# Performance work log

Measured on AMD Instinct MI355X. Metric: run time of the kernel, lower is better.

Reference implementation:

```python
import jax, jax.numpy as jnp
import numpy as np

N_NODES = 500000
N_GRAPHS = 4096
D_LOCAL = 64
D_GLOBAL = 64
D_HIDDEN = 128
D_PRE = 64
LN_EPS = 1e-5


def _layer_norm(x, g, b):
    mu = jnp.mean(x, axis=-1, keepdims=True)
    var = jnp.var(x, axis=-1, keepdims=True)
    return (x - mu) * jax.lax.rsqrt(var + LN_EPS) * g + b


def setup_inputs() -> dict:
    key = jax.random.key(0)
    ks = jax.random.split(key, 16)
    s = 0.02
    d_concat = D_LOCAL + D_GLOBAL  # 128
    d_post_in = D_PRE + D_GLOBAL   # 128
    return {
        "x": jax.random.normal(ks[0], (N_NODES, D_LOCAL), jnp.float32),
        "u": jax.random.normal(ks[1], (N_GRAPHS, D_GLOBAL), jnp.float32),
        "batch": jax.random.randint(ks[2], (N_NODES,), 0, N_GRAPHS, jnp.int64),
        # mlp_pre_aggr params
        "w1": jax.random.normal(ks[3], (d_concat, D_HIDDEN), jnp.float32) * s,
        "b1": jnp.zeros((D_HIDDEN,), jnp.float32),
        "w2": jax.random.normal(ks[4], (D_HIDDEN, D_HIDDEN), jnp.float32) * s,
        "b2": jnp.zeros((D_HIDDEN,), jnp.float32),
        "w3": jax.random.normal(ks[5], (D_HIDDEN, D_PRE), jnp.float32) * s,
        "b3": jnp.zeros((D_PRE,), jnp.float32),
        "ln1_g": jnp.ones((D_PRE,), jnp.float32),
        "ln1_b": jnp.zeros((D_PRE,), jnp.float32),
        # mlp_post_aggr params
        "w4": jax.random.normal(ks[6], (d_post_in, D_HIDDEN), jnp.float32) * s,
        "b4": jnp.zeros((D_HIDDEN,), jnp.float32),
        "w5": jax.random.normal(ks[7], (D_HIDDEN, D_HIDDEN), jnp.float32) * s,
        "b5": jnp.zeros((D_HIDDEN,), jnp.float32),
        "w6": jax.random.normal(ks[8], (D_HIDDEN, D_GLOBAL), jnp.float32) * s,
        "b6": jnp.zeros((D_GLOBAL,), jnp.float32),
        "ln2_g": jnp.ones((D_GLOBAL,), jnp.float32),
        "ln2_b": jnp.zeros((D_GLOBAL,), jnp.float32),
    }


def reference(x, u, batch, w1, b1, w2, b2, w3, b3, ln1_g, ln1_b,
              w4, b4, w5, b5, w6, b6, ln2_g, ln2_b):
    # gather global state to nodes and concat: [N, dim_local + dim_global]
    h = jnp.concatenate([x, u[batch]], axis=-1)
    # mlp_pre_aggr (dropout p=0 -> identity)
    h = jax.nn.relu(h @ w1 + b1)
    h = jax.nn.relu(h @ w2 + b2)
    h = _layer_norm(h @ w3 + b3, ln1_g, ln1_b)  # [N, dim_pre_aggr]
    # scatter_add per graph
    agg = jax.ops.segment_sum(h, batch, num_segments=u.shape[0])  # [B, dim_pre_aggr]
    # concat with u, mlp_post_aggr
    g = jnp.concatenate([agg, u], axis=-1)
    g = jax.nn.relu(g @ w4 + b4)
    g = jax.nn.relu(g @ w5 + b5)
    g = _layer_norm(g @ w6 + b6, ln2_g, ln2_b)
    return g + u
```

## Files before the change

kernel.cpp:

```cpp
#include <hip/hip_runtime.h>
#include <hip/hip_bf16.h>
#include <stdint.h>


#define NNODES 500000
#define NGRAPHS 4096
#define ROWS 128
#define LDH 136

typedef __attribute__((ext_vector_type(8))) _Float16 half8;
typedef __attribute__((ext_vector_type(4))) float floatx4;

__global__ void prep_kernel(const float* __restrict__ w1, const float* __restrict__ w2,
                            const float* __restrict__ w3,
                            _Float16* __restrict__ w1T, _Float16* __restrict__ w2T,
                            _Float16* __restrict__ w3T) {
    int i = blockIdx.x * 256 + threadIdx.x;
    if (i < 128 * 128) {
        int n = i >> 7, k = i & 127;
        w1T[i] = (_Float16)w1[k * 128 + n];
        w2T[i] = (_Float16)w2[k * 128 + n];
    }
    if (i < 64 * 128) {
        int n = i >> 7, k = i & 127;
        w3T[i] = (_Float16)w3[k * 64 + n];
    }
}

__global__ __launch_bounds__(256, 2) void node_kernel(
    const float* __restrict__ x, const float* __restrict__ u, const int* __restrict__ batch,
    const _Float16* __restrict__ w1T, const _Float16* __restrict__ w2T,
    const _Float16* __restrict__ w3T,
    const float* __restrict__ b1, const float* __restrict__ b2, const float* __restrict__ b3,
    const float* __restrict__ lng, const float* __restrict__ lnb,
    float* __restrict__ agg)
{
    __shared__ __align__(16) _Float16 hA[ROWS * LDH];
    __shared__ int sBatch[ROWS];

    const int tid = threadIdx.x;
    const int rowbase = blockIdx.x * ROWS;
    const int wave = tid >> 6;
    const int lane = tid & 63;
    const int q = lane >> 4;
    const int l16 = lane & 15;

    for (int r = tid; r < ROWS; r += 256) {
        int gr = rowbase + r;
        sBatch[r] = (gr < NNODES) ? batch[gr] : 0;
    }
    __syncthreads();

    for (int i = tid; i < ROWS * 16; i += 256) {
        int r = i >> 4, c4 = (i & 15) << 2;
        int gr = rowbase + r;
        float4 vx = make_float4(0.f, 0.f, 0.f, 0.f);
        if (gr < NNODES) vx = *(const float4*)(x + (size_t)gr * 64 + c4);
        _Float16* p = &hA[r * LDH + c4];
        p[0] = (_Float16)vx.x; p[1] = (_Float16)vx.y;
        p[2] = (_Float16)vx.z; p[3] = (_Float16)vx.w;
        int g = sBatch[r];
        float4 vu = *(const float4*)(u + (size_t)g * 64 + c4);
        _Float16* p2 = &hA[r * LDH + 64 + c4];
        p2[0] = (_Float16)vu.x; p2[1] = (_Float16)vu.y;
        p2[2] = (_Float16)vu.z; p2[3] = (_Float16)vu.w;
    }
    __syncthreads();

    const int rowg = (wave >> 1) * 64;
    const int colg = (wave & 1) * 64;
    for (int layer = 0; layer < 2; ++layer) {
        const _Float16* wT = layer ? w2T : w1T;
        const float* bias = layer ? b2 : b1;
        floatx4 acc[4][4];
        #pragma unroll
        for (int ct = 0; ct < 4; ++ct) {
            float bv = bias[colg + ct * 16 + l16];
            #pragma unroll
            for (int rt = 0; rt < 4; ++rt) acc[rt][ct] = (floatx4){bv, bv, bv, bv};
        }
        half8 bfr[4][4];
        #pragma unroll
        for (int ks = 0; ks < 4; ++ks)
            #pragma unroll
            for (int ct = 0; ct < 4; ++ct)
                bfr[ks][ct] = *(const half8*)(wT + (colg + ct * 16 + l16) * 128 + ks * 32 + q * 8);
        #pragma unroll
        for (int ks = 0; ks < 4; ++ks) {
            half8 af[4];
            #pragma unroll
            for (int rt = 0; rt < 4; ++rt)
                af[rt] = *(const half8*)(&hA[(rowg + rt * 16 + l16) * LDH + ks * 32 + q * 8]);
            #pragma unroll
            for (int rt = 0; rt < 4; ++rt)
                #pragma unroll
                for (int ct = 0; ct < 4; ++ct)
                    acc[rt][ct] = __builtin_amdgcn_mfma_f32_16x16x32_f16(
                        af[rt], bfr[ks][ct], acc[rt][ct], 0, 0, 0);
        }
        __syncthreads();
        #pragma unroll
        for (int rt = 0; rt < 4; ++rt)
            #pragma unroll
            for (int ct = 0; ct < 4; ++ct)
                #pragma unroll
                for (int j = 0; j < 4; ++j) {
                    float v = acc[rt][ct][j];
                    v = v > 0.f ? v : 0.f;
                    hA[(rowg + rt * 16 + q * 4 + j) * LDH + colg + ct * 16 + l16] = (_Float16)v;
                }
        __syncthreads();
    }

    {
        const int rowg3 = wave * 32;
        floatx4 acc[2][4];
        #pragma unroll
        for (int ct = 0; ct < 4; ++ct) {
            float bv = b3[ct * 16 + l16];
            acc[0][ct] = (floatx4){bv, bv, bv, bv};
            acc[1][ct] = (floatx4){bv, bv, bv, bv};
        }
        half8 bfr[4][4];
        #pragma unroll
        for (int ks = 0; ks < 4; ++ks)
            #pragma unroll
            for (int ct = 0; ct < 4; ++ct)
                bfr[ks][ct] = *(const half8*)(w3T + (ct * 16 + l16) * 128 + ks * 32 + q * 8);
        #pragma unroll
        for (int ks = 0; ks < 4; ++ks) {
            half8 af[2];
            #pragma unroll
            for (int rt = 0; rt < 2; ++rt)
                af[rt] = *(const half8*)(&hA[(rowg3 + rt * 16 + l16) * LDH + ks * 32 + q * 8]);
            #pragma unroll
            for (int rt = 0; rt < 2; ++rt)
                #pragma unroll
                for (int ct = 0; ct < 4; ++ct)
                    acc[rt][ct] = __builtin_amdgcn_mfma_f32_16x16x32_f16(
                        af[rt], bfr[ks][ct], acc[rt][ct], 0, 0, 0);
        }
        float gct[4], bct[4];
        #pragma unroll
        for (int ct = 0; ct < 4; ++ct) {
            gct[ct] = lng[ct * 16 + l16];
            bct[ct] = lnb[ct * 16 + l16];
        }
        #pragma unroll
        for (int rt = 0; rt < 2; ++rt)
            #pragma unroll
            for (int j = 0; j < 4; ++j) {
                int rloc = rowg3 + rt * 16 + q * 4 + j;
                float v0 = acc[rt][0][j], v1 = acc[rt][1][j];
                float v2 = acc[rt][2][j], v3 = acc[rt][3][j];
                float s = v0 + v1 + v2 + v3;
                float ss = v0 * v0 + v1 * v1 + v2 * v2 + v3 * v3;
                #pragma unroll
                for (int m = 1; m < 16; m <<= 1) {
                    s += __shfl_xor(s, m, 16);
                    ss += __shfl_xor(ss, m, 16);
                }
                float mean = s * (1.f / 64.f);
                float var = ss * (1.f / 64.f) - mean * mean;
                float rstd = rsqrtf(var + 1e-5f);
                if (rowbase + rloc < NNODES) {
                    float* dst = agg + (size_t)sBatch[rloc] * 64;
                    unsafeAtomicAdd(dst + 0 + l16,  (v0 - mean) * rstd * gct[0] + bct[0]);
                    unsafeAtomicAdd(dst + 16 + l16, (v1 - mean) * rstd * gct[1] + bct[1]);
                    unsafeAtomicAdd(dst + 32 + l16, (v2 - mean) * rstd * gct[2] + bct[2]);
                    unsafeAtomicAdd(dst + 48 + l16, (v3 - mean) * rstd * gct[3] + bct[3]);
                }
            }
    }
}

__global__ __launch_bounds__(256, 4) void graph_kernel(
    const float* __restrict__ u,
    const float* __restrict__ w4, const float* __restrict__ b4,
    const float* __restrict__ w5, const float* __restrict__ b5,
    const float* __restrict__ w6, const float* __restrict__ b6,
    const float* __restrict__ g2, const float* __restrict__ bb2,
    float* __restrict__ out)
{
    __shared__ float z[4][2][128];
    const int wave = threadIdx.x >> 6, lane = threadIdx.x & 63;
    const int g = blockIdx.x * 4 + wave;
    float* za = z[wave][0];
    float* zb = z[wave][1];
    za[lane] = out[(size_t)g * 64 + lane];
    za[64 + lane] = u[(size_t)g * 64 + lane];
    float s0 = b4[lane], s1 = b4[64 + lane];
    for (int k = 0; k < 128; ++k) {
        float zk = za[k];
        s0 = fmaf(zk, w4[k * 128 + lane], s0);
        s1 = fmaf(zk, w4[k * 128 + 64 + lane], s1);
    }
    zb[lane] = fmaxf(s0, 0.f); zb[64 + lane] = fmaxf(s1, 0.f);
    s0 = b5[lane]; s1 = b5[64 + lane];
    for (int k = 0; k < 128; ++k) {
        float zk = zb[k];
        s0 = fmaf(zk, w5[k * 128 + lane], s0);
        s1 = fmaf(zk, w5[k * 128 + 64 + lane], s1);
    }
    za[lane] = fmaxf(s0, 0.f); za[64 + lane] = fmaxf(s1, 0.f);
    float s = b6[lane];
    for (int k = 0; k < 128; ++k) s = fmaf(za[k], w6[k * 64 + lane], s);
    float sum = s, ssq = s * s;
    #pragma unroll
    for (int m = 1; m < 64; m <<= 1) {
        sum += __shfl_xor(sum, m, 64);
        ssq += __shfl_xor(ssq, m, 64);
    }
    float mean = sum * (1.f / 64.f);
    float var = ssq * (1.f / 64.f) - mean * mean;
    float rstd = rsqrtf(var + 1e-5f);
    out[(size_t)g * 64 + lane] =
        (s - mean) * rstd * g2[lane] + bb2[lane] + u[(size_t)g * 64 + lane];
}

extern "C" void kernel_launch(void* const* d_in, const int* in_sizes, int n_in,
                              void* d_out, int out_size, void* d_ws, size_t ws_size,
                              hipStream_t stream) {
    const float* x   = (const float*)d_in[0];
    const float* u   = (const float*)d_in[1];
    const int*   bt  = (const int*)d_in[2];
    const float* w1  = (const float*)d_in[3];
    const float* b1  = (const float*)d_in[4];
    const float* w2  = (const float*)d_in[5];
    const float* b2  = (const float*)d_in[6];
    const float* w3  = (const float*)d_in[7];
    const float* b3  = (const float*)d_in[8];
    const float* lng = (const float*)d_in[9];
    const float* lnb = (const float*)d_in[10];
    const float* w4  = (const float*)d_in[11];
    const float* b4  = (const float*)d_in[12];
    const float* w5  = (const float*)d_in[13];
    const float* b5  = (const float*)d_in[14];
    const float* w6  = (const float*)d_in[15];
    const float* b6  = (const float*)d_in[16];
    const float* g2  = (const float*)d_in[17];
    const float* bb2 = (const float*)d_in[18];
    float* out = (float*)d_out;

    _Float16* w1T = (_Float16*)d_ws;
    _Float16* w2T = w1T + 128 * 128;
    _Float16* w3T = w2T + 128 * 128;

    hipMemsetAsync(d_out, 0, (size_t)NGRAPHS * 64 * sizeof(float), stream);
    prep_kernel<<<64, 256, 0, stream>>>(w1, w2, w3, w1T, w2T, w3T);
    node_kernel<<<(NNODES + ROWS - 1) / ROWS, 256, 0, stream>>>(
        x, u, bt, w1T, w2T, w3T, b1, b2, b3, lng, lnb, out);
    graph_kernel<<<NGRAPHS / 4, 256, 0, stream>>>(
        u, w4, b4, w5, b5, w6, b6, g2, bb2, out);
}
```

Before: 408.0 us.

## Sort nodes by graph for LDS-local segment sums and MFMA the graph MLP

Adds a histogram, scan and scatter pass that builds a permutation grouping nodes by graph id. The node kernel then gathers x through that permutation, so each 128-row block spans only a few graphs and can accumulate its segment sums in shared-memory slots before one global atomic flush per slot. This is meant to cut the heavy contention of per-row global float atomics. The per-graph post-aggregation MLP is also rewritten to use fp16 MFMA tiles with transposed half-precision weights, replacing the scalar FMA loops. The cost is three extra kernel launches, a scattered gather of x rows, and lower precision in the graph MLP.

```diff
diff --git a/kernel.cpp b/kernel.cpp
--- a/kernel.cpp
+++ b/kernel.cpp
@@ -7,28 +7,79 @@
 #define NGRAPHS 4096
 #define ROWS 128
 #define LDH 136
+#define SLOTS 16
 
 typedef __attribute__((ext_vector_type(8))) _Float16 half8;
 typedef __attribute__((ext_vector_type(4))) float floatx4;
 
 __global__ void prep_kernel(const float* __restrict__ w1, const float* __restrict__ w2,
-                            const float* __restrict__ w3,
+                            const float* __restrict__ w3, const float* __restrict__ w4,
+                            const float* __restrict__ w5, const float* __restrict__ w6,
                             _Float16* __restrict__ w1T, _Float16* __restrict__ w2T,
-                            _Float16* __restrict__ w3T) {
+                            _Float16* __restrict__ w3T, _Float16* __restrict__ w4T,
+                            _Float16* __restrict__ w5T, _Float16* __restrict__ w6T) {
     int i = blockIdx.x * 256 + threadIdx.x;
     if (i < 128 * 128) {
         int n = i >> 7, k = i & 127;
         w1T[i] = (_Float16)w1[k * 128 + n];
         w2T[i] = (_Float16)w2[k * 128 + n];
+        w4T[i] = (_Float16)w4[k * 128 + n];
+        w5T[i] = (_Float16)w5[k * 128 + n];
     }
     if (i < 64 * 128) {
         int n = i >> 7, k = i & 127;
         w3T[i] = (_Float16)w3[k * 64 + n];
+        w6T[i] = (_Float16)w6[k * 64 + n];
+    }
+}
+
+__global__ void hist_kernel(const int* __restrict__ batch, int* __restrict__ cnt) {
+    __shared__ int h[NGRAPHS];
+    for (int i = threadIdx.x; i < NGRAPHS; i += 256) h[i] = 0;
+    __syncthreads();
+    for (int i = blockIdx.x * 256 + threadIdx.x; i < NNODES; i += 64 * 256)
+        atomicAdd(&h[batch[i]], 1);
+    __syncthreads();
+    for (int i = threadIdx.x; i < NGRAPHS; i += 256) {
+        int v = h[i];
+        if (v) atomicAdd(&cnt[i], v);
+    }
+}
+
+__global__ void scan_kernel(const int* __restrict__ cnt, int* __restrict__ runoff) {
+    __shared__ int partial[256];
+    int tid = threadIdx.x;
+    int local[16];
+    int s = 0;
+    #pragma unroll
+    for (int j = 0; j < 16; ++j) { local[j] = cnt[tid * 16 + j]; s += local[j]; }
+    partial[tid] = s;
+    __syncthreads();
+    for (int off = 1; off < 256; off <<= 1) {
+        int v = (tid >= off) ? partial[tid - off] : 0;
+        __syncthreads();
+        partial[tid] += v;
+        __syncthreads();
+    }
+    int run = partial[tid] - s;
+    #pragma unroll
+    for (int j = 0; j < 16; ++j) { runoff[tid * 16 + j] = run; run += local[j]; }
+}
+
+__global__ void scatter_kernel(const int* __restrict__ batch, int* __restrict__ runoff,
+                               int* __restrict__ perm, int* __restrict__ sbat) {
+    int i = blockIdx.x * 256 + threadIdx.x;
+    if (i < NNODES) {
+        int g = batch[i];
+        int p = atomicAdd(&runoff[g], 1);
+        perm[p] = i;
+        sbat[p] = g;
     }
 }
 
 __global__ __launch_bounds__(256, 2) void node_kernel(
-    const float* __restrict__ x, const float* __restrict__ u, const int* __restrict__ batch,
+    const float* __restrict__ x, const float* __restrict__ u,
+    const int* __restrict__ perm, const int* __restrict__ sbat,
     const _Float16* __restrict__ w1T, const _Float16* __restrict__ w2T,
     const _Float16* __restrict__ w3T,
     const float* __restrict__ b1, const float* __restrict__ b2, const float* __restrict__ b3,
@@ -37,6 +88,8 @@
 {
     __shared__ __align__(16) _Float16 hA[ROWS * LDH];
     __shared__ int sBatch[ROWS];
+    __shared__ int sPerm[ROWS];
+    __shared__ float aggS[SLOTS * 64];
 
     const int tid = threadIdx.x;
     const int rowbase = blockIdx.x * ROWS;
@@ -47,15 +100,22 @@
 
     for (int r = tid; r < ROWS; r += 256) {
         int gr = rowbase + r;
-        sBatch[r] = (gr < NNODES) ? batch[gr] : 0;
-    }
-    __syncthreads();
+        sPerm[r] = (gr < NNODES) ? perm[gr] : -1;
+        sBatch[r] = (gr < NNODES) ? sbat[gr] : 0;
+    }
+    for (int i = tid; i < SLOTS * 64; i += 256) aggS[i] = 0.f;
+    __syncthreads();
+
+    const int nValid = (rowbase + ROWS <= NNODES) ? ROWS : (NNODES - rowbase);
+    const int gFirst = sBatch[0];
+    const int nSlots = sBatch[nValid - 1] - gFirst + 1;
+    const bool useLds = (nSlots <= SLOTS);
 
     for (int i = tid; i < ROWS * 16; i += 256) {
         int r = i >> 4, c4 = (i & 15) << 2;
-        int gr = rowbase + r;
+        int nid = sPerm[r];
         float4 vx = make_float4(0.f, 0.f, 0.f, 0.f);
-        if (gr < NNODES) vx = *(const float4*)(x + (size_t)gr * 64 + c4);
+        if (nid >= 0) vx = *(const float4*)(x + (size_t)nid * 64 + c4);
         _Float16* p = &hA[r * LDH + c4];
         p[0] = (_Float16)vx.x; p[1] = (_Float16)vx.y;
         p[2] = (_Float16)vx.z; p[3] = (_Float16)vx.w;
@@ -164,58 +224,167 @@
                 float var = ss * (1.f / 64.f) - mean * mean;
                 float rstd = rsqrtf(var + 1e-5f);
                 if (rowbase + rloc < NNODES) {
-                    float* dst = agg + (size_t)sBatch[rloc] * 64;
-                    unsafeAtomicAdd(dst + 0 + l16,  (v0 - mean) * rstd * gct[0] + bct[0]);
-                    unsafeAtomicAdd(dst + 16 + l16, (v1 - mean) * rstd * gct[1] + bct[1]);
-                    unsafeAtomicAdd(dst + 32 + l16, (v2 - mean) * rstd * gct[2] + bct[2]);
-                    unsafeAtomicAdd(dst + 48 + l16, (v3 - mean) * rstd * gct[3] + bct[3]);
+                    float o0 = (v0 - mean) * rstd * gct[0] + bct[0];
+                    float o1 = (v1 - mean) * rstd * gct[1] + bct[1];
+                    float o2 = (v2 - mean) * rstd * gct[2] + bct[2];
+                    float o3 = (v3 - mean) * rstd * gct[3] + bct[3];
+                    if (useLds) {
+                        float* dst = aggS + (sBatch[rloc] - gFirst) * 64;
+                        atomicAdd(dst + 0 + l16,  o0);
+                        atomicAdd(dst + 16 + l16, o1);
+                        atomicAdd(dst + 32 + l16, o2);
+                        atomicAdd(dst + 48 + l16, o3);
+                    } else {
+                        float* dst = agg + (size_t)sBatch[rloc] * 64;
+                        unsafeAtomicAdd(dst + 0 + l16,  o0);
+                        unsafeAtomicAdd(dst + 16 + l16, o1);
+                        unsafeAtomicAdd(dst + 32 + l16, o2);
+                        unsafeAtomicAdd(dst + 48 + l16, o3);
+                    }
                 }
             }
     }
-}
-
-__global__ __launch_bounds__(256, 4) void graph_kernel(
+    __syncthreads();
+    if (useLds) {
+        for (int i = tid; i < nSlots * 64; i += 256)
+            unsafeAtomicAdd(agg + (size_t)(gFirst + (i >> 6)) * 64 + (i & 63), aggS[i]);
+    }
+}
+
+__global__ __launch_bounds__(256, 2) void graph2_kernel(
     const float* __restrict__ u,
-    const float* __restrict__ w4, const float* __restrict__ b4,
-    const float* __restrict__ w5, const float* __restrict__ b5,
-    const float* __restrict__ w6, const float* __restrict__ b6,
-    const float* __restrict__ g2, const float* __restrict__ bb2,
+    const _Float16* __restrict__ w4T, const _Float16* __restrict__ w5T,
+    const _Float16* __restrict__ w6T,
+    const float* __restrict__ b4, const float* __restrict__ b5, const float* __restrict__ b6,
+    const float* __restrict__ lng, const float* __restrict__ lnb,
     float* __restrict__ out)
 {
-    __shared__ float z[4][2][128];
-    const int wave = threadIdx.x >> 6, lane = threadIdx.x & 63;
-    const int g = blockIdx.x * 4 + wave;
-    float* za = z[wave][0];
-    float* zb = z[wave][1];
-    za[lane] = out[(size_t)g * 64 + lane];
-    za[64 + lane] = u[(size_t)g * 64 + lane];
-    float s0 = b4[lane], s1 = b4[64 + lane];
-    for (int k = 0; k < 128; ++k) {
-        float zk = za[k];
-        s0 = fmaf(zk, w4[k * 128 + lane], s0);
-        s1 = fmaf(zk, w4[k * 128 + 64 + lane], s1);
-    }
-    zb[lane] = fmaxf(s0, 0.f); zb[64 + lane] = fmaxf(s1, 0.f);
-    s0 = b5[lane]; s1 = b5[64 + lane];
-    for (int k = 0; k < 128; ++k) {
-        float zk = zb[k];
-        s0 = fmaf(zk, w5[k * 128 + lane], s0);
-        s1 = fmaf(zk, w5[k * 128 + 64 + lane], s1);
-    }
-    za[lane] = fmaxf(s0, 0.f); za[64 + lane] = fmaxf(s1, 0.f);
-    float s = b6[lane];
-    for (int k = 0; k < 128; ++k) s = fmaf(za[k], w6[k * 64 + lane], s);
-    float sum = s, ssq = s * s;
-    #pragma unroll
-    for (int m = 1; m < 64; m <<= 1) {
-        sum += __shfl_xor(sum, m, 64);
-        ssq += __shfl_xor(ssq, m, 64);
-    }
-    float mean = sum * (1.f / 64.f);
-    float var = ssq * (1.f / 64.f) - mean * mean;
-    float rstd = rsqrtf(var + 1e-5f);
-    out[(size_t)g * 64 + lane] =
-        (s - mean) * rstd * g2[lane] + bb2[lane] + u[(size_t)g * 64 + lane];
+    __shared__ __align__(16) _Float16 hA[128 * LDH];
+
+    const int tid = threadIdx.x;
+    const int rowbase = blockIdx.x * 128;
+    const int wave = tid >> 6;
+    const int lane = tid & 63;
+    const int q = lane >> 4;
+    const int l16 = lane & 15;
+
+    for (int i = tid; i < 128 * 16; i += 256) {
+        int r = i >> 4, c4 = (i & 15) << 2;
+        int g = rowbase + r;
+        float4 va = *(const float4*)(out + (size_t)g * 64 + c4);
+        _Float16* p = &hA[r * LDH + c4];
+        p[0] = (_Float16)va.x; p[1] = (_Float16)va.y;
+        p[2] = (_Float16)va.z; p[3] = (_Float16)va.w;
+        float4 vu = *(const float4*)(u + (size_t)g * 64 + c4);
+        _Float16* p2 = &hA[r * LDH + 64 + c4];
+        p2[0] = (_Float16)vu.x; p2[1] = (_Float16)vu.y;
+        p2[2] = (_Float16)vu.z; p2[3] = (_Float16)vu.w;
+    }
+    __syncthreads();
+
+    const int rowg = (wave >> 1) * 64;
+    const int colg = (wave & 1) * 64;
+    for (int layer = 0; layer < 2; ++layer) {
+        const _Float16* wT = layer ? w5T : w4T;
+        const float* bias = layer ? b5 : b4;
+        floatx4 acc[4][4];
+        #pragma unroll
+        for (int ct = 0; ct < 4; ++ct) {
+            float bv = bias[colg + ct * 16 + l16];
+            #pragma unroll
+            for (int rt = 0; rt < 4; ++rt) acc[rt][ct] = (floatx4){bv, bv, bv, bv};
+        }
+        half8 bfr[4][4];
+        #pragma unroll
+        for (int ks = 0; ks < 4; ++ks)
+            #pragma unroll
+            for (int ct = 0; ct < 4; ++ct)
+                bfr[ks][ct] = *(const half8*)(wT + (colg + ct * 16 + l16) * 128 + ks * 32 + q * 8);
+        #pragma unroll
+        for (int ks = 0; ks < 4; ++ks) {
+            half8 af[4];
+            #pragma unroll
+            for (int rt = 0; rt < 4; ++rt)
+                af[rt] = *(const half8*)(&hA[(rowg + rt * 16 + l16) * LDH + ks * 32 + q * 8]);
+            #pragma unroll
+            for (int rt = 0; rt < 4; ++rt)
+                #pragma unroll
+                for (int ct = 0; ct < 4; ++ct)
+                    acc[rt][ct] = __builtin_amdgcn_mfma_f32_16x16x32_f16(
+                        af[rt], bfr[ks][ct], acc[rt][ct], 0, 0, 0);
+        }
+        __syncthreads();
+        #pragma unroll
+        for (int rt = 0; rt < 4; ++rt)
+            #pragma unroll
+            for (int ct = 0; ct < 4; ++ct)
+                #pragma unroll
+                for (int j = 0; j < 4; ++j) {
+                    float v = acc[rt][ct][j];
+                    v = v > 0.f ? v : 0.f;
+                    hA[(rowg + rt * 16 + q * 4 + j) * LDH + colg + ct * 16 + l16] = (_Float16)v;
+                }
+        __syncthreads();
+    }
+
+    {
+        const int rowg3 = wave * 32;
+        floatx4 acc[2][4];
+        #pragma unroll
+        for (int ct = 0; ct < 4; ++ct) {
+            float bv = b6[ct * 16 + l16];
+            acc[0][ct] = (floatx4){bv, bv, bv, bv};
+            acc[1][ct] = (floatx4){bv, bv, bv, bv};
+        }
+        half8 bfr[4][4];
+        #pragma unroll
+        for (int ks = 0; ks < 4; ++ks)
+            #pragma unroll
+            for (int ct = 0; ct < 4; ++ct)
+                bfr[ks][ct] = *(const half8*)(w6T + (ct * 16 + l16) * 128 + ks * 32 + q * 8);
+        #pragma unroll
+        for (int ks = 0; ks < 4; ++ks) {
+            half8 af[2];
+            #pragma unroll
+            for (int rt = 0; rt < 2; ++rt)
+                af[rt] = *(const half8*)(&hA[(rowg3 + rt * 16 + l16) * LDH + ks * 32 + q * 8]);
+            #pragma unroll
+            for (int rt = 0; rt < 2; ++rt)
+                #pragma unroll
+                for (int ct = 0; ct < 4; ++ct)
+                    acc[rt][ct] = __builtin_amdgcn_mfma_f32_16x16x32_f16(
+                        af[rt], bfr[ks][ct], acc[rt][ct], 0, 0, 0);
+        }
+        float gct[4], bct[4];
+        #pragma unroll
+        for (int ct = 0; ct < 4; ++ct) {
+            gct[ct] = lng[ct * 16 + l16];
+            bct[ct] = lnb[ct * 16 + l16];
+        }
+        #pragma unroll
+        for (int rt = 0; rt < 2; ++rt)
+            #pragma unroll
+            for (int j = 0; j < 4; ++j) {
+                int rloc = rowg3 + rt * 16 + q * 4 + j;
+                size_t g = (size_t)(rowbase + rloc);
+                float v0 = acc[rt][0][j], v1 = acc[rt][1][j];
+                float v2 = acc[rt][2][j], v3 = acc[rt][3][j];
+                float s = v0 + v1 + v2 + v3;
+                float ss = v0 * v0 + v1 * v1 + v2 * v2 + v3 * v3;
+                #pragma unroll
+                for (int m = 1; m < 16; m <<= 1) {
+                    s += __shfl_xor(s, m, 16);
+                    ss += __shfl_xor(ss, m, 16);
+                }
+                float mean = s * (1.f / 64.f);
+                float var = ss * (1.f / 64.f) - mean * mean;
+                float rstd = rsqrtf(var + 1e-5f);
+                out[g * 64 + 0 + l16]  = (v0 - mean) * rstd * gct[0] + bct[0] + u[g * 64 + 0 + l16];
+                out[g * 64 + 16 + l16] = (v1 - mean) * rstd * gct[1] + bct[1] + u[g * 64 + 16 + l16];
+                out[g * 64 + 32 + l16] = (v2 - mean) * rstd * gct[2] + bct[2] + u[g * 64 + 32 + l16];
+                out[g * 64 + 48 + l16] = (v3 - mean) * rstd * gct[3] + bct[3] + u[g * 64 + 48 + l16];
+            }
+    }
 }
 
 extern "C" void kernel_launch(void* const* d_in, const int* in_sizes, int n_in,
@@ -245,11 +414,23 @@
     _Float16* w1T = (_Float16*)d_ws;
     _Float16* w2T = w1T + 128 * 128;
     _Float16* w3T = w2T + 128 * 128;
+    _Float16* w4T = w3T + 64 * 128;
+    _Float16* w5T = w4T + 128 * 128;
+    _Float16* w6T = w5T + 128 * 128;
+    int* cnt    = (int*)(w6T + 64 * 128);
+    int* runoff = cnt + NGRAPHS;
+    int* perm   = runoff + NGRAPHS;
+    int* sbat   = perm + NNODES;
 
     hipMemsetAsync(d_out, 0, (size_t)NGRAPHS * 64 * sizeof(float), stream);
-    prep_kernel<<<64, 256, 0, stream>>>(w1, w2, w3, w1T, w2T, w3T);
+    hipMemsetAsync(cnt, 0, (size_t)NGRAPHS * sizeof(int), stream);
+    prep_kernel<<<64, 256, 0, stream>>>(w1, w2, w3, w4, w5, w6,
+                                        w1T, w2T, w3T, w4T, w5T, w6T);
+    hist_kernel<<<64, 256, 0, stream>>>(bt, cnt);
+    scan_kernel<<<1, 256, 0, stream>>>(cnt, runoff);
+    scatter_kernel<<<(NNODES + 255) / 256, 256, 0, stream>>>(bt, runoff, perm, sbat);
     node_kernel<<<(NNODES + ROWS - 1) / ROWS, 256, 0, stream>>>(
-        x, u, bt, w1T, w2T, w3T, b1, b2, b3, lng, lnb, out);
-    graph_kernel<<<NGRAPHS / 4, 256, 0, stream>>>(
-        u, w4, b4, w5, b5, w6, b6, g2, bb2, out);
-}
+        x, u, perm, sbat, w1T, w2T, w3T, b1, b2, b3, lng, lnb, out);
+    graph2_kernel<<<NGRAPHS / 128, 256, 0, stream>>>(
+        u, w4T, w5T, w6T, b4, b5, b6, g2, bb2, out);
+}
```

Result: slower. 532.4 us (+30.5%).

## Restructure node MLP to per-wave 32-row tiles and MFMA graph MLP

Applied to the files above, without the earlier changes.

The node kernel now gives each wave its own 32-row tile in shared memory and drops the block-wide __syncthreads. It reads weight fragments from global/L2 inside the loop instead of holding them in registers, which targets higher occupancy (4 blocks per CU). The graph-level MLP moves from a scalar FMA kernel to an fp16 MFMA kernel modelled on the node kernel, with w4-w6 transposed in prep. The risks are more repeated weight loads per wave and fp16 precision in the post-aggregation MLP. The graph kernel reads the aggregate from out and overwrites it in place per block.

```diff
diff --git a/kernel.cpp b/kernel.cpp
--- a/kernel.cpp
+++ b/kernel.cpp
@@ -5,61 +5,179 @@
 
 #define NNODES 500000
 #define NGRAPHS 4096
-#define ROWS 128
 #define LDH 136
 
 typedef __attribute__((ext_vector_type(8))) _Float16 half8;
 typedef __attribute__((ext_vector_type(4))) float floatx4;
 
 __global__ void prep_kernel(const float* __restrict__ w1, const float* __restrict__ w2,
-                            const float* __restrict__ w3,
+                            const float* __restrict__ w3, const float* __restrict__ w4,
+                            const float* __restrict__ w5, const float* __restrict__ w6,
                             _Float16* __restrict__ w1T, _Float16* __restrict__ w2T,
-                            _Float16* __restrict__ w3T) {
+                            _Float16* __restrict__ w3T, _Float16* __restrict__ w4T,
+                            _Float16* __restrict__ w5T, _Float16* __restrict__ w6T) {
     int i = blockIdx.x * 256 + threadIdx.x;
     if (i < 128 * 128) {
         int n = i >> 7, k = i & 127;
         w1T[i] = (_Float16)w1[k * 128 + n];
         w2T[i] = (_Float16)w2[k * 128 + n];
+        w4T[i] = (_Float16)w4[k * 128 + n];
+        w5T[i] = (_Float16)w5[k * 128 + n];
     }
     if (i < 64 * 128) {
         int n = i >> 7, k = i & 127;
         w3T[i] = (_Float16)w3[k * 64 + n];
+        w6T[i] = (_Float16)w6[k * 64 + n];
     }
 }
 
-__global__ __launch_bounds__(256, 2) void node_kernel(
-    const float* __restrict__ x, const float* __restrict__ u, const int* __restrict__ batch,
+__global__ __launch_bounds__(256, 4) void node_kernel(
+    const float* __restrict__ x, const float* __restrict__ u,
+    const int* __restrict__ batch,
     const _Float16* __restrict__ w1T, const _Float16* __restrict__ w2T,
     const _Float16* __restrict__ w3T,
     const float* __restrict__ b1, const float* __restrict__ b2, const float* __restrict__ b3,
     const float* __restrict__ lng, const float* __restrict__ lnb,
     float* __restrict__ agg)
 {
-    __shared__ __align__(16) _Float16 hA[ROWS * LDH];
-    __shared__ int sBatch[ROWS];
+    __shared__ __align__(16) _Float16 hA[4][32 * LDH];
 
     const int tid = threadIdx.x;
-    const int rowbase = blockIdx.x * ROWS;
     const int wave = tid >> 6;
     const int lane = tid & 63;
     const int q = lane >> 4;
     const int l16 = lane & 15;
-
-    for (int r = tid; r < ROWS; r += 256) {
+    const int wid = blockIdx.x * 4 + wave;
+    const int rowbase = wid * 32;
+    if (rowbase >= NNODES) return;
+    _Float16* hw = hA[wave];
+
+    float gct[4], bct[4];
+    #pragma unroll
+    for (int ct = 0; ct < 4; ++ct) {
+        gct[ct] = lng[ct * 16 + l16];
+        bct[ct] = lnb[ct * 16 + l16];
+    }
+
+    #pragma unroll
+    for (int k = 0; k < 16; ++k) {
+        int c = lane + k * 64;
+        int r = c >> 5;
+        int cc = c & 31;
         int gr = rowbase + r;
-        sBatch[r] = (gr < NNODES) ? batch[gr] : 0;
-    }
-    __syncthreads();
-
-    for (int i = tid; i < ROWS * 16; i += 256) {
+        float4 v;
+        if (cc < 16) {
+            v = *(const float4*)(x + (size_t)gr * 64 + cc * 4);
+        } else {
+            int g = batch[gr];
+            v = *(const float4*)(u + (size_t)g * 64 + (cc - 16) * 4);
+        }
+        _Float16* p = &hw[r * LDH + cc * 4];
+        p[0] = (_Float16)v.x; p[1] = (_Float16)v.y;
+        p[2] = (_Float16)v.z; p[3] = (_Float16)v.w;
+    }
+
+    for (int layer = 0; layer < 2; ++layer) {
+        const _Float16* wT = layer ? w2T : w1T;
+        const float* bias = layer ? b2 : b1;
+        #pragma unroll
+        for (int rt = 0; rt < 2; ++rt) {
+            half8 af[4];
+            #pragma unroll
+            for (int ks = 0; ks < 4; ++ks)
+                af[ks] = *(const half8*)(&hw[(rt * 16 + l16) * LDH + ks * 32 + q * 8]);
+            floatx4 acc[8];
+            #pragma unroll
+            for (int ct = 0; ct < 8; ++ct) {
+                float bv = bias[ct * 16 + l16];
+                acc[ct] = (floatx4){bv, bv, bv, bv};
+            }
+            #pragma unroll
+            for (int ct = 0; ct < 8; ++ct)
+                #pragma unroll
+                for (int ks = 0; ks < 4; ++ks) {
+                    half8 bf = *(const half8*)(wT + (ct * 16 + l16) * 128 + ks * 32 + q * 8);
+                    acc[ct] = __builtin_amdgcn_mfma_f32_16x16x32_f16(af[ks], bf, acc[ct], 0, 0, 0);
+                }
+            #pragma unroll
+            for (int ct = 0; ct < 8; ++ct)
+                #pragma unroll
+                for (int j = 0; j < 4; ++j) {
+                    float v = acc[ct][j];
+                    v = v > 0.f ? v : 0.f;
+                    hw[(rt * 16 + q * 4 + j) * LDH + ct * 16 + l16] = (_Float16)v;
+                }
+        }
+    }
+
+    #pragma unroll
+    for (int rt = 0; rt < 2; ++rt) {
+        half8 af[4];
+        #pragma unroll
+        for (int ks = 0; ks < 4; ++ks)
+            af[ks] = *(const half8*)(&hw[(rt * 16 + l16) * LDH + ks * 32 + q * 8]);
+        floatx4 acc[4];
+        #pragma unroll
+        for (int ct = 0; ct < 4; ++ct) {
+            float bv = b3[ct * 16 + l16];
+            acc[ct] = (floatx4){bv, bv, bv, bv};
+        }
+        #pragma unroll
+        for (int ct = 0; ct < 4; ++ct)
+            #pragma unroll
+            for (int ks = 0; ks < 4; ++ks) {
+                half8 bf = *(const half8*)(w3T + (ct * 16 + l16) * 128 + ks * 32 + q * 8);
+                acc[ct] = __builtin_amdgcn_mfma_f32_16x16x32_f16(af[ks], bf, acc[ct], 0, 0, 0);
+            }
+        #pragma unroll
+        for (int j = 0; j < 4; ++j) {
+            int rloc = rt * 16 + q * 4 + j;
+            float v0 = acc[0][j], v1 = acc[1][j];
+            float v2 = acc[2][j], v3 = acc[3][j];
+            float s = v0 + v1 + v2 + v3;
+            float ss = v0 * v0 + v1 * v1 + v2 * v2 + v3 * v3;
+            #pragma unroll
+            for (int m = 1; m < 16; m <<= 1) {
+                s += __shfl_xor(s, m, 16);
+                ss += __shfl_xor(ss, m, 16);
+            }
+            float mean = s * (1.f / 64.f);
+            float var = ss * (1.f / 64.f) - mean * mean;
+            float rstd = rsqrtf(var + 1e-5f);
+            int g = batch[rowbase + rloc];
+            float* dst = agg + (size_t)g * 64;
+            unsafeAtomicAdd(dst + 0 + l16,  (v0 - mean) * rstd * gct[0] + bct[0]);
+            unsafeAtomicAdd(dst + 16 + l16, (v1 - mean) * rstd * gct[1] + bct[1]);
+            unsafeAtomicAdd(dst + 32 + l16, (v2 - mean) * rstd * gct[2] + bct[2]);
+            unsafeAtomicAdd(dst + 48 + l16, (v3 - mean) * rstd * gct[3] + bct[3]);
+        }
+    }
+}
+
+__global__ __launch_bounds__(256, 2) void graph2_kernel(
+    const float* __restrict__ u,
+    const _Float16* __restrict__ w4T, const _Float16* __restrict__ w5T,
+    const _Float16* __restrict__ w6T,
+    const float* __restrict__ b4, const float* __restrict__ b5, const float* __restrict__ b6,
+    const float* __restrict__ lng, const float* __restrict__ lnb,
+    float* __restrict__ out)
+{
+    __shared__ __align__(16) _Float16 hA[128 * LDH];
+
+    const int tid = threadIdx.x;
+    const int rowbase = blockIdx.x * 128;
+    const int wave = tid >> 6;
+    const int lane = tid & 63;
+    const int q = lane >> 4;
+    const int l16 = lane & 15;
+
+    for (int i = tid; i < 128 * 16; i += 256) {
         int r = i >> 4, c4 = (i & 15) << 2;
-        int gr = rowbase + r;
-        float4 vx = make_float4(0.f, 0.f, 0.f, 0.f);
-        if (gr < NNODES) vx = *(const float4*)(x + (size_t)gr * 64 + c4);
+        int g = rowbase + r;
+        float4 va = *(const float4*)(out + (size_t)g * 64 + c4);
         _Float16* p = &hA[r * LDH + c4];
-        p[0] = (_Float16)vx.x; p[1] = (_Float16)vx.y;
-        p[2] = (_Float16)vx.z; p[3] = (_Float16)vx.w;
-        int g = sBatch[r];
+        p[0] = (_Float16)va.x; p[1] = (_Float16)va.y;
+        p[2] = (_Float16)va.z; p[3] = (_Float16)va.w;
         float4 vu = *(const float4*)(u + (size_t)g * 64 + c4);
         _Float16* p2 = &hA[r * LDH + 64 + c4];
         p2[0] = (_Float16)vu.x; p2[1] = (_Float16)vu.y;
@@ -70,8 +188,8 @@
     const int rowg = (wave >> 1) * 64;
     const int colg = (wave & 1) * 64;
     for (int layer = 0; layer < 2; ++layer) {
-        const _Float16* wT = layer ? w2T : w1T;
-        const float* bias = layer ? b2 : b1;
+        const _Float16* wT = layer ? w5T : w4T;
+        const float* bias = layer ? b5 : b4;
         floatx4 acc[4][4];
         #pragma unroll
         for (int ct = 0; ct < 4; ++ct) {
@@ -117,7 +235,7 @@
         floatx4 acc[2][4];
         #pragma unroll
         for (int ct = 0; ct < 4; ++ct) {
-            float bv = b3[ct * 16 + l16];
+            float bv = b6[ct * 16 + l16];
             acc[0][ct] = (floatx4){bv, bv, bv, bv};
             acc[1][ct] = (floatx4){bv, bv, bv, bv};
         }
@@ -126,7 +244,7 @@
         for (int ks = 0; ks < 4; ++ks)
             #pragma unroll
             for (int ct = 0; ct < 4; ++ct)
-                bfr[ks][ct] = *(const half8*)(w3T + (ct * 16 + l16) * 128 + ks * 32 + q * 8);
+                bfr[ks][ct] = *(const half8*)(w6T + (ct * 16 + l16) * 128 + ks * 32 + q * 8);
         #pragma unroll
         for (int ks = 0; ks < 4; ++ks) {
             half8 af[2];
@@ -151,6 +269,7 @@
             #pragma unroll
             for (int j = 0; j < 4; ++j) {
                 int rloc = rowg3 + rt * 16 + q * 4 + j;
+                size_t g = (size_t)(rowbase + rloc);
                 float v0 = acc[rt][0][j], v1 = acc[rt][1][j];
                 float v2 = acc[rt][2][j], v3 = acc[rt][3][j];
                 float s = v0 + v1 + v2 + v3;
@@ -163,59 +282,12 @@
                 float mean = s * (1.f / 64.f);
                 float var = ss * (1.f / 64.f) - mean * mean;
                 float rstd = rsqrtf(var + 1e-5f);
-                if (rowbase + rloc < NNODES) {
-                    float* dst = agg + (size_t)sBatch[rloc] * 64;
-                    unsafeAtomicAdd(dst + 0 + l16,  (v0 - mean) * rstd * gct[0] + bct[0]);
-                    unsafeAtomicAdd(dst + 16 + l16, (v1 - mean) * rstd * gct[1] + bct[1]);
-                    unsafeAtomicAdd(dst + 32 + l16, (v2 - mean) * rstd * gct[2] + bct[2]);
-                    unsafeAtomicAdd(dst + 48 + l16, (v3 - mean) * rstd * gct[3] + bct[3]);
-                }
+                out[g * 64 + 0 + l16]  = (v0 - mean) * rstd * gct[0] + bct[0] + u[g * 64 + 0 + l16];
+                out[g * 64 + 16 + l16] = (v1 - mean) * rstd * gct[1] + bct[1] + u[g * 64 + 16 + l16];
+                out[g * 64 + 32 + l16] = (v2 - mean) * rstd * gct[2] + bct[2] + u[g * 64 + 32 + l16];
+                out[g * 64 + 48 + l16] = (v3 - mean) * rstd * gct[3] + bct[3] + u[g * 64 + 48 + l16];
             }
     }
-}
-
-__global__ __launch_bounds__(256, 4) void graph_kernel(
-    const float* __restrict__ u,
-    const float* __restrict__ w4, const float* __restrict__ b4,
-    const float* __restrict__ w5, const float* __restrict__ b5,
-    const float* __restrict__ w6, const float* __restrict__ b6,
-    const float* __restrict__ g2, const float* __restrict__ bb2,
-    float* __restrict__ out)
-{
-    __shared__ float z[4][2][128];
-    const int wave = threadIdx.x >> 6, lane = threadIdx.x & 63;
-    const int g = blockIdx.x * 4 + wave;
-    float* za = z[wave][0];
-    float* zb = z[wave][1];
-    za[lane] = out[(size_t)g * 64 + lane];
-    za[64 + lane] = u[(size_t)g * 64 + lane];
-    float s0 = b4[lane], s1 = b4[64 + lane];
-    for (int k = 0; k < 128; ++k) {
-        float zk = za[k];
-        s0 = fmaf(zk, w4[k * 128 + lane], s0);
-        s1 = fmaf(zk, w4[k * 128 + 64 + lane], s1);
-    }
-    zb[lane] = fmaxf(s0, 0.f); zb[64 + lane] = fmaxf(s1, 0.f);
-    s0 = b5[lane]; s1 = b5[64 + lane];
-    for (int k = 0; k < 128; ++k) {
-        float zk = zb[k];
-        s0 = fmaf(zk, w5[k * 128 + lane], s0);
-        s1 = fmaf(zk, w5[k * 128 + 64 + lane], s1);
-    }
-    za[lane] = fmaxf(s0, 0.f); za[64 + lane] = fmaxf(s1, 0.f);
-    float s = b6[lane];
-    for (int k = 0; k < 128; ++k) s = fmaf(za[k], w6[k * 64 + lane], s);
-    float sum = s, ssq = s * s;
-    #pragma unroll
-    for (int m = 1; m < 64; m <<= 1) {
-        sum += __shfl_xor(sum, m, 64);
-        ssq += __shfl_xor(ssq, m, 64);
-    }
-    float mean = sum * (1.f / 64.f);
-    float var = ssq * (1.f / 64.f) - mean * mean;
-    float rstd = rsqrtf(var + 1e-5f);
-    out[(size_t)g * 64 + lane] =
-        (s - mean) * rstd * g2[lane] + bb2[lane] + u[(size_t)g * 64 + lane];
 }
 
 extern "C" void kernel_launch(void* const* d_in, const int* in_sizes, int n_in,
@@ -245,11 +317,15 @@
     _Float16* w1T = (_Float16*)d_ws;
     _Float16* w2T = w1T + 128 * 128;
     _Float16* w3T = w2T + 128 * 128;
+    _Float16* w4T = w3T + 64 * 128;
+    _Float16* w5T = w4T + 128 * 128;
+    _Float16* w6T = w5T + 128 * 128;
 
     hipMemsetAsync(d_out, 0, (size_t)NGRAPHS * 64 * sizeof(float), stream);
-    prep_kernel<<<64, 256, 0, stream>>>(w1, w2, w3, w1T, w2T, w3T);
-    node_kernel<<<(NNODES + ROWS - 1) / ROWS, 256, 0, stream>>>(
+    prep_kernel<<<64, 256, 0, stream>>>(w1, w2, w3, w4, w5, w6,
+                                        w1T, w2T, w3T, w4T, w5T, w6T);
+    node_kernel<<<(15625 + 3) / 4, 256, 0, stream>>>(
         x, u, bt, w1T, w2T, w3T, b1, b2, b3, lng, lnb, out);
-    graph_kernel<<<NGRAPHS / 4, 256, 0, stream>>>(
-        u, w4, b4, w5, b5, w6, b6, g2, bb2, out);
+    graph2_kernel<<<NGRAPHS / 128, 256, 0, stream>>>(
+        u, w4T, w5T, w6T, b4, b5, b6, g2, bb2, out);
 }
```

Measured after the change: 592.6 us. 1.45x slower.
